# Optimization experiments

Hardware: AMD Instinct MI355X
Metric: run time of the kernel (lower is better)

## Reference

```python
import jax, jax.numpy as jnp
import numpy as np

B, N, F, E, D, H, L = 4, 2048, 2, 16, 32, 4, 2
GRAPH_LAYERS = 3
FLOW_ITERS = 10
COST_C = 1.0        # quadratic cost: c*x^2, inv_derivative(y) = y/(2c)
BIG_NUMBER = 1e7


def setup_inputs():
    key = jax.random.key(0)
    ks = jax.random.split(key, 20)
    node_features = jax.random.normal(ks[0], (B, N, F), jnp.float32)
    node_embeddings = jax.random.normal(ks[1], (B, N, E), jnp.float32)
    demands = jax.random.normal(ks[2], (B, N, 1), jnp.float32)
    demands = demands - demands.mean(axis=1, keepdims=True)  # flow conservation
    adj = (jax.random.uniform(ks[3], (B, N, N)) < 0.01).astype(jnp.float32)
    adj = adj * (1.0 - jnp.eye(N, dtype=jnp.float32))
    eye = jnp.broadcast_to(jnp.eye(N, dtype=jnp.float32), (B, N, N))
    neighborhoods = jnp.stack([eye, adj], axis=1)  # [B,L,N,N] hop-0 and hop-1
    def g(k, shape):
        return jax.random.normal(k, shape, jnp.float32) * 0.1
    params = {
        'We1': g(ks[4], (E + F, D)), 'be1': jnp.zeros((D,), jnp.float32),
        'We2': g(ks[5], (D, D)), 'be2': jnp.zeros((D,), jnp.float32),
        'w_attn': g(ks[6], (H, D)),
        'Wo': g(ks[7], (D, D)), 'bo': jnp.zeros((D,), jnp.float32),
        'Wz': g(ks[8], (D, D)), 'Uz': g(ks[9], (D, D)), 'bz': jnp.zeros((D,), jnp.float32),
        'Wr': g(ks[10], (D, D)), 'Ur': g(ks[11], (D, D)), 'br': jnp.zeros((D,), jnp.float32),
        'Wh': g(ks[12], (D, D)), 'Uh': g(ks[13], (D, D)), 'bh': jnp.zeros((D,), jnp.float32),
        'Wd1': g(ks[14], (D, D)), 'bd1': jnp.zeros((D,), jnp.float32),
        'Wd2': g(ks[15], (D, 1)), 'bd2': jnp.zeros((1,), jnp.float32),
        'Wv1': g(ks[16], (D, D)), 'bv1': jnp.zeros((D,), jnp.float32),
        'Wv2': g(ks[17], (D, 1)), 'bv2': jnp.zeros((1,), jnp.float32),
    }
    return {'node_features': node_features, 'node_embeddings': node_embeddings,
            'demands': demands, 'adj': adj, 'neighborhoods': neighborhoods, **params}


def _forward(node_features, node_embeddings, demands, adj, neighborhoods,
             We1, be1, We2, be2, w_attn, Wo, bo,
             Wz, Uz, bz, Wr, Ur, br, Wh, Uh, bh,
             Wd1, bd1, Wd2, bd2, Wv1, bv1, Wv2, bv2):
    # --- node encoder MLP (tanh, activate_final=True) ---
    x = jnp.concatenate([node_embeddings, node_features], axis=-1)   # [B,N,E+F]
    enc = jnp.tanh(jnp.tanh(x @ We1 + be1) @ We2 + be2)               # [B,N,D]
    # row-normalized neighborhood operators (degree-normalized aggregation)
    Mnorm = neighborhoods / (jnp.sum(neighborhoods, axis=-1, keepdims=True) + 1.0)
    # --- graph_layers x (attention neighborhood + GRU state update) ---
    for _ in range(GRAPH_LAYERS):
        agg = jnp.einsum('blnm,bmd->blnd', Mnorm, enc)                # [B,L,N,D]
        scores = jnp.einsum('blnd,hd->bhnl', jnp.tanh(agg), w_attn)   # [B,H,N,L]
        alpha = jax.nn.softmax(scores, axis=-1)
        ctx = jnp.einsum('bhnl,blnd->bnd', alpha, agg) / H            # mean over heads
        nbr = jnp.tanh(ctx @ Wo + bo)                                 # [B,N,D]
        z = jax.nn.sigmoid(nbr @ Wz + enc @ Uz + bz)
        r = jax.nn.sigmoid(nbr @ Wr + enc @ Ur + br)
        h = jnp.tanh(nbr @ Wh + (r * enc) @ Uh + bh)
        enc = z * enc + (1.0 - z) * h
    # --- primal: edge weights, masked softmax, proportional flow solver ---
    pred = (enc @ Wd1 + bd1) @ Wd2 + bd2                              # [B,N,1]
    pw = pred * jnp.transpose(pred, (0, 2, 1))                        # [B,N,N]
    weights = -BIG_NUMBER * (1.0 - adj) + pw
    fwp = jax.nn.softmax(weights, axis=-1)                            # rows sum to 1
    flow0 = fwp * jax.nn.relu(-demands)

    def step(flow, _):
        inflow = jnp.sum(flow, axis=1)[..., None]                     # [B,N,1]
        return fwp * jax.nn.relu(inflow - demands), None

    flow, _ = jax.lax.scan(step, flow0, None, length=FLOW_ITERS)
    flow_cost = jnp.sum(COST_C * flow * flow, axis=(1, 2))            # [B]
    # --- dual: dual variables, dual flows via inverse cost derivative ---
    dual = (enc @ Wv1 + bv1) @ Wv2 + bv2                              # [B,N,1]
    dd = dual - jnp.transpose(dual, (0, 2, 1))                        # [B,N,N]
    df = adj * jax.nn.relu(dd / (2.0 * COST_C))
    dual_cost = jnp.sum(COST_C * df * df - dd * df, axis=(1, 2)) \
        - jnp.sum(dual * demands, axis=(1, 2))                        # [B]
    return flow_cost - dual_cost                                      # primal-dual gap loss, [B]


def reference(node_features, node_embeddings, demands, adj, neighborhoods,
              We1, be1, We2, be2, w_attn, Wo, bo,
              Wz, Uz, bz, Wr, Ur, br, Wh, Uh, bh,
              Wd1, bd1, Wd2, bd2, Wv1, bv1, Wv2, bv2):
    return _forward(node_features, node_embeddings, demands, adj, neighborhoods,
                    We1, be1, We2, be2, w_attn, Wo, bo,
                    Wz, Uz, bz, Wr, Ur, br, Wh, Uh, bh,
                    Wd1, bd1, Wd2, bd2, Wv1, bv1, Wv2, bv2)
```

## Files before the change

kernel.cpp:

```cpp
#include <hip/hip_runtime.h>

#define NN 2048
#define NB 4
#define BN (NB * NN)
#define MAXD 96

__global__ __launch_bounds__(256) void k_front(
    const float* __restrict__ feat, const float* __restrict__ emb,
    const float* __restrict__ We1, const float* __restrict__ be1,
    const float* __restrict__ We2, const float* __restrict__ be2,
    float* __restrict__ enc_out,
    const float* __restrict__ adj, int* __restrict__ deg, int* __restrict__ cols,
    int* __restrict__ tdeg)
{
    int tid = threadIdx.x;
    if (blockIdx.x < 1024) {
        __shared__ float sW1[18 * 32], sb1[32], sW2[32 * 32], sb2[32];
        for (int i = tid; i < 18 * 32; i += 256) sW1[i] = We1[i];
        for (int i = tid; i < 32 * 32; i += 256) sW2[i] = We2[i];
        if (tid < 32) { sb1[tid] = be1[tid]; sb2[tid] = be2[tid]; }
        __syncthreads();
        int group = tid >> 5, j = tid & 31;
        int node = blockIdx.x * 8 + group;
        float x;
        if (j < 16)      x = emb[node * 16 + j];
        else if (j < 18) x = feat[node * 2 + (j - 16)];
        else             x = 0.f;
        float acc = sb1[j];
#pragma unroll
        for (int k = 0; k < 18; k++)
            acc += __shfl(x, k, 32) * sW1[k * 32 + j];
        float h = tanhf(acc);
        float acc2 = sb2[j];
#pragma unroll
        for (int k = 0; k < 32; k++)
            acc2 += __shfl(h, k, 32) * sW2[k * 32 + j];
        enc_out[node * 32 + j] = tanhf(acc2);
    } else {
        int wave = tid >> 6, lane = tid & 63;
        int row = (blockIdx.x - 1024) * 4 + wave;
        const float4* p = (const float4*)(adj + (size_t)row * NN);
        int cnt = 0;
        int base = row * MAXD;
#pragma unroll
        for (int it = 0; it < 8; it++) {
            float4 v = p[it * 64 + lane];
            float va[4] = { v.x, v.y, v.z, v.w };
#pragma unroll
            for (int c = 0; c < 4; c++) {
                unsigned long long m = __ballot(va[c] != 0.f);
                if (va[c] != 0.f) {
                    int pos = cnt + __popcll(m & ((1ull << lane) - 1ull));
                    if (pos < MAXD) cols[base + pos] = it * 256 + lane * 4 + c;
                }
                cnt += __popcll(m);
            }
        }
        if (lane == 0) {
            deg[row] = cnt < MAXD ? cnt : MAXD;
            tdeg[row] = 0;
        }
    }
}

__device__ __forceinline__ float layer_body(
    int node, int j, int d, const int* __restrict__ cp,
    const float* __restrict__ encB, float e,
    const float* sAttn, const float* sWo, const float* sbo,
    const float* sWz, const float* sUz, const float* sbz,
    const float* sWr, const float* sUr, const float* sbr,
    const float* sWh, const float* sUh, const float* sbh)
{
    float agg0 = 0.5f * e;
    int iA = cp[j];
    int iB = cp[j + 32];
    float a1 = 0.f, a1b = 0.f;
    int dmin = d < 32 ? d : 32;
#pragma unroll 4
    for (int i = 0; i < dmin - 1; i += 2) {
        int m0 = __shfl(iA, i, 32);
        int m1 = __shfl(iA, i + 1, 32);
        a1  += encB[m0 * 32 + j];
        a1b += encB[m1 * 32 + j];
    }
    if (dmin & 1) { int m = __shfl(iA, dmin - 1, 32); a1 += encB[m * 32 + j]; }
#pragma unroll 2
    for (int i = 32; i < d; i++) {
        int m = __shfl(iB, i - 32, 32);
        a1 += encB[m * 32 + j];
    }
    a1 = (a1 + a1b) * (1.0f / (float)(d + 1));
    float t0 = tanhf(agg0), t1 = tanhf(a1);
    float sc[8];
#pragma unroll
    for (int h2 = 0; h2 < 4; h2++) { sc[h2] = sAttn[h2 * 32 + j] * t0; sc[4 + h2] = sAttn[h2 * 32 + j] * t1; }
#pragma unroll
    for (int off = 16; off >= 1; off >>= 1)
#pragma unroll
        for (int q = 0; q < 8; q++) sc[q] += __shfl_xor(sc[q], off, 32);
    float c0 = 0.f, c1 = 0.f;
#pragma unroll
    for (int h2 = 0; h2 < 4; h2++) {
        float a = sc[h2], bsc = sc[4 + h2];
        float mx = fmaxf(a, bsc);
        float e0 = expf(a - mx), e1 = expf(bsc - mx);
        float inv = 1.0f / (e0 + e1);
        c0 += e0 * inv; c1 += e1 * inv;
    }
    c0 *= 0.25f; c1 *= 0.25f;
    float ctx = c0 * agg0 + c1 * a1;
    float acc = sbo[j];
#pragma unroll
    for (int k = 0; k < 32; k++) acc += __shfl(ctx, k, 32) * sWo[k * 32 + j];
    float nbr = tanhf(acc);
    float az = sbz[j], ar = sbr[j], ah = sbh[j];
#pragma unroll
    for (int k = 0; k < 32; k++) {
        float nb = __shfl(nbr, k, 32);
        float en = __shfl(e, k, 32);
        az += nb * sWz[k * 32 + j] + en * sUz[k * 32 + j];
        ar += nb * sWr[k * 32 + j] + en * sUr[k * 32 + j];
        ah += nb * sWh[k * 32 + j];
    }
    float z = 1.0f / (1.0f + expf(-az));
    float r = 1.0f / (1.0f + expf(-ar));
    float re = r * e;
#pragma unroll
    for (int k = 0; k < 32; k++) ah += __shfl(re, k, 32) * sUh[k * 32 + j];
    float hc = tanhf(ah);
    return z * e + (1.0f - z) * hc;
}

__global__ __launch_bounds__(1024) void k_layer(
    const float* __restrict__ enc_in, float* __restrict__ enc_out,
    const int* __restrict__ deg, const int* __restrict__ cols,
    const float* __restrict__ w_attn,
    const float* __restrict__ Wo, const float* __restrict__ bo,
    const float* __restrict__ Wz, const float* __restrict__ Uz, const float* __restrict__ bz,
    const float* __restrict__ Wr, const float* __restrict__ Ur, const float* __restrict__ br,
    const float* __restrict__ Wh, const float* __restrict__ Uh, const float* __restrict__ bh)
{
    __shared__ float sWo[1024], sWz[1024], sUz[1024], sWr[1024], sUr[1024], sWh[1024], sUh[1024];
    __shared__ float sbo[32], sbz[32], sbr[32], sbh[32], sAttn[128];
    int tid = threadIdx.x;
    {
        int i = tid;
        sWo[i] = Wo[i]; sWz[i] = Wz[i]; sUz[i] = Uz[i];
        sWr[i] = Wr[i]; sUr[i] = Ur[i]; sWh[i] = Wh[i]; sUh[i] = Uh[i];
    }
    if (tid < 32) { sbo[tid] = bo[tid]; sbz[tid] = bz[tid]; sbr[tid] = br[tid]; sbh[tid] = bh[tid]; }
    if (tid < 128) sAttn[tid] = w_attn[tid];
    __syncthreads();
    int group = tid >> 5, j = tid & 31;
    int node = blockIdx.x * 32 + group;
    int b = node >> 11;
    const float* encB = enc_in + (size_t)(b * NN) * 32;
    float e = enc_in[node * 32 + j];
    int d = deg[node];
    const int* cp = cols + node * MAXD;
    float eo = layer_body(node, j, d, cp, encB, e, sAttn, sWo, sbo,
                          sWz, sUz, sbz, sWr, sUr, sbr, sWh, sUh, sbh);
    enc_out[node * 32 + j] = eo;
}

__global__ __launch_bounds__(1024) void k_layer_last(
    const float* __restrict__ enc_in,
    const int* __restrict__ deg, const int* __restrict__ cols,
    const float* __restrict__ w_attn,
    const float* __restrict__ Wo, const float* __restrict__ bo,
    const float* __restrict__ Wz, const float* __restrict__ Uz, const float* __restrict__ bz,
    const float* __restrict__ Wr, const float* __restrict__ Ur, const float* __restrict__ br,
    const float* __restrict__ Wh, const float* __restrict__ Uh, const float* __restrict__ bh,
    const float* __restrict__ Wd1, const float* __restrict__ bd1,
    const float* __restrict__ Wd2, const float* __restrict__ bd2,
    const float* __restrict__ Wv1, const float* __restrict__ bv1,
    const float* __restrict__ Wv2, const float* __restrict__ bv2,
    float* __restrict__ pred, float* __restrict__ dual)
{
    __shared__ float sWo[1024], sWz[1024], sUz[1024], sWr[1024], sUr[1024], sWh[1024], sUh[1024];
    __shared__ float sWd1[1024], sWv1[1024];
    __shared__ float sbo[32], sbz[32], sbr[32], sbh[32], sAttn[128];
    __shared__ float sbd1[32], sbv1[32], sWd2[32], sWv2[32];
    int tid = threadIdx.x;
    {
        int i = tid;
        sWo[i] = Wo[i]; sWz[i] = Wz[i]; sUz[i] = Uz[i];
        sWr[i] = Wr[i]; sUr[i] = Ur[i]; sWh[i] = Wh[i]; sUh[i] = Uh[i];
        sWd1[i] = Wd1[i]; sWv1[i] = Wv1[i];
    }
    if (tid < 32) {
        sbo[tid] = bo[tid]; sbz[tid] = bz[tid]; sbr[tid] = br[tid]; sbh[tid] = bh[tid];
        sbd1[tid] = bd1[tid]; sbv1[tid] = bv1[tid]; sWd2[tid] = Wd2[tid]; sWv2[tid] = Wv2[tid];
    }
    if (tid < 128) sAttn[tid] = w_attn[tid];
    __syncthreads();
    int group = tid >> 5, j = tid & 31;
    int node = blockIdx.x * 32 + group;
    int b = node >> 11;
    const float* encB = enc_in + (size_t)(b * NN) * 32;
    float e = enc_in[node * 32 + j];
    int d = deg[node];
    const int* cp = cols + node * MAXD;
    float eo = layer_body(node, j, d, cp, encB, e, sAttn, sWo, sbo,
                          sWz, sUz, sbz, sWr, sUr, sbr, sWh, sUh, sbh);
    float ad = sbd1[j], av = sbv1[j];
#pragma unroll
    for (int k = 0; k < 32; k++) {
        float en = __shfl(eo, k, 32);
        ad += en * sWd1[k * 32 + j];
        av += en * sWv1[k * 32 + j];
    }
    float pd = ad * sWd2[j];
    float dv = av * sWv2[j];
#pragma unroll
    for (int off = 16; off >= 1; off >>= 1) {
        pd += __shfl_xor(pd, off, 32);
        dv += __shfl_xor(dv, off, 32);
    }
    if (j == 0) {
        pred[node] = pd + bd2[0];
        dual[node] = dv + bv2[0];
    }
}

__global__ __launch_bounds__(256) void k_edge_scatter(
    const int* __restrict__ deg, const int* __restrict__ cols,
    const float* __restrict__ pred, const float* __restrict__ dual,
    int* __restrict__ tdeg, unsigned* __restrict__ tpack,
    float* __restrict__ rowsq, float* __restrict__ rowdual)
{
    int wave = threadIdx.x >> 6, lane = threadIdx.x & 63;
    int row = blockIdx.x * 4 + wave;
    int b = row >> 11;
    int rloc = row & (NN - 1);
    const float* predB = pred + b * NN;
    const float* dualB = dual + b * NN;
    int d = deg[row];
    int base = row * MAXD;
    float pn = pred[row];
    float dn = dual[row];
    float mx = -1e30f;
    for (int i = lane; i < d; i += 64) {
        int c = cols[base + i];
        mx = fmaxf(mx, pn * predB[c]);
    }
#pragma unroll
    for (int off = 32; off >= 1; off >>= 1) mx = fmaxf(mx, __shfl_xor(mx, off));
    float den = 0.f, du = 0.f;
    for (int i = lane; i < d; i += 64) {
        int c = cols[base + i];
        den += expf(pn * predB[c] - mx);
        float dd = dn - dualB[c];
        if (dd > 0.f) du -= 0.25f * dd * dd;
    }
#pragma unroll
    for (int off = 32; off >= 1; off >>= 1) { den += __shfl_xor(den, off); du += __shfl_xor(du, off); }
    float invden = 1.0f / den;
    float rs = 0.f;
    for (int i = lane; i < d; i += 64) {
        int c = cols[base + i];
        float f = expf(pn * predB[c] - mx) * invden;
        rs += f * f;
        int pos = atomicAdd(&tdeg[b * NN + c], 1);
        if (pos < MAXD) {
            unsigned wv = ((__float_as_uint(f) + 0x400u) & 0xFFFFF800u) | (unsigned)rloc;
            tpack[(size_t)(b * MAXD + pos) * NN + c] = wv;
        }
    }
#pragma unroll
    for (int off = 32; off >= 1; off >>= 1) rs += __shfl_xor(rs, off);
    if (lane == 0) { rowsq[row] = rs; rowdual[row] = du; }
}

__global__ __launch_bounds__(1024) void k_flow_batch(
    const int* __restrict__ tdeg, const unsigned* __restrict__ tpack,
    const float* __restrict__ demands,
    const float* __restrict__ rowsq, const float* __restrict__ rowdual,
    const float* __restrict__ dual, float* __restrict__ out)
{
    __shared__ float sdem[NN], sA[NN], sBuf[NN];
    __shared__ float red[3][16];
    int tid = threadIdx.x;
    int b = blockIdx.x;
    const float* demB = demands + b * NN;
    for (int n = tid; n < NN; n += 1024) {
        float dm = demB[n];
        sdem[n] = dm;
        sA[n] = fmaxf(-dm, 0.f);
    }
    __syncthreads();
    int n0 = tid, n1 = tid + 1024;
    int d0 = tdeg[b * NN + n0];
    int d1 = tdeg[b * NN + n1];
    const unsigned* tp = tpack + (size_t)b * MAXD * NN;
#pragma unroll 1
    for (int it = 0; it < 5; it++) {
        {
            float a0 = 0.f, a1 = 0.f;
            for (int i = 0; i < d0; i++) {
                unsigned wv = tp[i * NN + n0];
                a0 += __uint_as_float(wv & 0xFFFFF800u) * sA[wv & 0x7FFu];
            }
            for (int i = 0; i < d1; i++) {
                unsigned wv = tp[i * NN + n1];
                a1 += __uint_as_float(wv & 0xFFFFF800u) * sA[wv & 0x7FFu];
            }
            sBuf[n0] = fmaxf(a0 - sdem[n0], 0.f);
            sBuf[n1] = fmaxf(a1 - sdem[n1], 0.f);
        }
        __syncthreads();
        {
            float a0 = 0.f, a1 = 0.f;
            for (int i = 0; i < d0; i++) {
                unsigned wv = tp[i * NN + n0];
                a0 += __uint_as_float(wv & 0xFFFFF800u) * sBuf[wv & 0x7FFu];
            }
            for (int i = 0; i < d1; i++) {
                unsigned wv = tp[i * NN + n1];
                a1 += __uint_as_float(wv & 0xFFFFF800u) * sBuf[wv & 0x7FFu];
            }
            sA[n0] = fmaxf(a0 - sdem[n0], 0.f);
            sA[n1] = fmaxf(a1 - sdem[n1], 0.f);
        }
        __syncthreads();
    }
    float fc = 0.f, ds = 0.f, dq = 0.f;
    for (int n = tid; n < NN; n += 1024) {
        int row = b * NN + n;
        float sv = sA[n];
        fc += rowsq[row] * sv * sv;
        ds += rowdual[row];
        dq += dual[row] * sdem[n];
    }
#pragma unroll
    for (int off = 32; off >= 1; off >>= 1) {
        fc += __shfl_xor(fc, off);
        ds += __shfl_xor(ds, off);
        dq += __shfl_xor(dq, off);
    }
    int wv = tid >> 6;
    if ((tid & 63) == 0) { red[0][wv] = fc; red[1][wv] = ds; red[2][wv] = dq; }
    __syncthreads();
    if (tid == 0) {
        float a = 0.f, s1 = 0.f, s2 = 0.f;
        for (int w = 0; w < 16; w++) { a += red[0][w]; s1 += red[1][w]; s2 += red[2][w]; }
        out[b] = a - s1 + s2;
    }
}

extern "C" void kernel_launch(void* const* d_in, const int* in_sizes, int n_in,
                              void* d_out, int out_size, void* d_ws, size_t ws_size,
                              hipStream_t stream) {
    const float* feat = (const float*)d_in[0];
    const float* emb  = (const float*)d_in[1];
    const float* dem  = (const float*)d_in[2];
    const float* adj  = (const float*)d_in[3];
    const float* We1 = (const float*)d_in[5];
    const float* be1 = (const float*)d_in[6];
    const float* We2 = (const float*)d_in[7];
    const float* be2 = (const float*)d_in[8];
    const float* w_attn = (const float*)d_in[9];
    const float* Wo = (const float*)d_in[10];
    const float* bo = (const float*)d_in[11];
    const float* Wz = (const float*)d_in[12];
    const float* Uz = (const float*)d_in[13];
    const float* bz = (const float*)d_in[14];
    const float* Wr = (const float*)d_in[15];
    const float* Ur = (const float*)d_in[16];
    const float* br = (const float*)d_in[17];
    const float* Wh = (const float*)d_in[18];
    const float* Uh = (const float*)d_in[19];
    const float* bh = (const float*)d_in[20];
    const float* Wd1 = (const float*)d_in[21];
    const float* bd1 = (const float*)d_in[22];
    const float* Wd2 = (const float*)d_in[23];
    const float* bd2 = (const float*)d_in[24];
    const float* Wv1 = (const float*)d_in[25];
    const float* bv1 = (const float*)d_in[26];
    const float* Wv2 = (const float*)d_in[27];
    const float* bv2 = (const float*)d_in[28];
    float* out = (float*)d_out;

    float* w = (float*)d_ws;
    float* enc0 = w;            w += (size_t)BN * 32;
    float* enc1 = w;            w += (size_t)BN * 32;
    int*   degp = (int*)w;      w += BN;
    int*   colp = (int*)w;      w += (size_t)BN * MAXD;
    float* pred = w;            w += BN;
    float* dual = w;            w += BN;
    float* rowsq = w;           w += BN;
    float* rowdual = w;         w += BN;
    int*   tdeg = (int*)w;      w += BN;
    unsigned* tpk = (unsigned*)w; w += (size_t)BN * MAXD;

    k_front<<<3072, 256, 0, stream>>>(feat, emb, We1, be1, We2, be2, enc0,
                                      adj, degp, colp, tdeg);
    k_layer<<<BN / 32, 1024, 0, stream>>>(enc0, enc1, degp, colp, w_attn,
                                          Wo, bo, Wz, Uz, bz, Wr, Ur, br, Wh, Uh, bh);
    k_layer<<<BN / 32, 1024, 0, stream>>>(enc1, enc0, degp, colp, w_attn,
                                          Wo, bo, Wz, Uz, bz, Wr, Ur, br, Wh, Uh, bh);
    k_layer_last<<<BN / 32, 1024, 0, stream>>>(enc0, degp, colp, w_attn,
                                               Wo, bo, Wz, Uz, bz, Wr, Ur, br, Wh, Uh, bh,
                                               Wd1, bd1, Wd2, bd2, Wv1, bv1, Wv2, bv2,
                                               pred, dual);
    k_edge_scatter<<<BN / 4, 256, 0, stream>>>(degp, colp, pred, dual,
                                               tdeg, tpk, rowsq, rowdual);
    k_flow_batch<<<NB, 1024, 0, stream>>>(tdeg, tpk, dem,
                                          rowsq, rowdual, dual, out);
}
```

Baseline: 406.8 us.

## Use fast math intrinsics, sigmoid-form attention, and packed shared-memory weights in GNN layers

Replaces tanhf/expf/division with exp-based tanh, __expf and hardware reciprocal throughout. Rewrites the two-way attention softmax as a sigmoid of the score difference, which halves the reductions. Broadcasts neighbour indices, context and gate inputs through shared memory instead of wave shuffles, and packs the GRU weights into float4/float2 so fewer LDS loads are needed. The cost is lower numerical accuracy from the approximate math and extra shared-memory traffic and footprint per block.

```diff
diff --git a/kernel.cpp b/kernel.cpp
--- a/kernel.cpp
+++ b/kernel.cpp
@@ -4,6 +4,16 @@
 #define NB 4
 #define BN (NB * NN)
 #define MAXD 96
+
+__device__ __forceinline__ float fast_rcp(float x) { return __builtin_amdgcn_rcpf(x); }
+__device__ __forceinline__ float fast_tanh(float x) {
+    float a = __expf(2.0f * fabsf(x));
+    float r = 1.0f - 2.0f * fast_rcp(1.0f + a);
+    return copysignf(r, x);
+}
+__device__ __forceinline__ float fast_sigmoid(float x) {
+    return fast_rcp(1.0f + __expf(-x));
+}
 
 __global__ __launch_bounds__(256) void k_front(
     const float* __restrict__ feat, const float* __restrict__ emb,
@@ -30,12 +40,12 @@
 #pragma unroll
         for (int k = 0; k < 18; k++)
             acc += __shfl(x, k, 32) * sW1[k * 32 + j];
-        float h = tanhf(acc);
+        float h = fast_tanh(acc);
         float acc2 = sb2[j];
 #pragma unroll
         for (int k = 0; k < 32; k++)
             acc2 += __shfl(h, k, 32) * sW2[k * 32 + j];
-        enc_out[node * 32 + j] = tanhf(acc2);
+        enc_out[node * 32 + j] = fast_tanh(acc2);
     } else {
         int wave = tid >> 6, lane = tid & 63;
         int row = (blockIdx.x - 1024) * 4 + wave;
@@ -63,71 +73,66 @@
     }
 }
 
-__device__ __forceinline__ float layer_body(
-    int node, int j, int d, const int* __restrict__ cp,
+__device__ __forceinline__ float layer_body2(
+    int g, int j, int d, const int* __restrict__ cp,
     const float* __restrict__ encB, float e,
-    const float* sAttn, const float* sWo, const float* sbo,
-    const float* sWz, const float* sUz, const float* sbz,
-    const float* sWr, const float* sUr, const float* sbr,
-    const float* sWh, const float* sUh, const float* sbh)
-{
-    float agg0 = 0.5f * e;
-    int iA = cp[j];
-    int iB = cp[j + 32];
+    const float4* sPack, const float2* sWhUh, const float* sWo,
+    const float* sAttn, const float* sbo, const float* sbz,
+    const float* sbr, const float* sbh,
+    int (*sCols)[64], float2 (*sNE)[32], float (*sCtx)[32])
+{
+    sCols[g][j]      = cp[j];
+    sCols[g][j + 32] = cp[j + 32];
     float a1 = 0.f, a1b = 0.f;
-    int dmin = d < 32 ? d : 32;
-#pragma unroll 4
-    for (int i = 0; i < dmin - 1; i += 2) {
-        int m0 = __shfl(iA, i, 32);
-        int m1 = __shfl(iA, i + 1, 32);
+    int i = 0;
+#pragma unroll 2
+    for (; i + 1 < d; i += 2) {
+        int m0 = sCols[g][i], m1 = sCols[g][i + 1];
         a1  += encB[m0 * 32 + j];
         a1b += encB[m1 * 32 + j];
     }
-    if (dmin & 1) { int m = __shfl(iA, dmin - 1, 32); a1 += encB[m * 32 + j]; }
-#pragma unroll 2
-    for (int i = 32; i < d; i++) {
-        int m = __shfl(iB, i - 32, 32);
-        a1 += encB[m * 32 + j];
-    }
-    a1 = (a1 + a1b) * (1.0f / (float)(d + 1));
-    float t0 = tanhf(agg0), t1 = tanhf(a1);
-    float sc[8];
-#pragma unroll
-    for (int h2 = 0; h2 < 4; h2++) { sc[h2] = sAttn[h2 * 32 + j] * t0; sc[4 + h2] = sAttn[h2 * 32 + j] * t1; }
-#pragma unroll
-    for (int off = 16; off >= 1; off >>= 1)
-#pragma unroll
-        for (int q = 0; q < 8; q++) sc[q] += __shfl_xor(sc[q], off, 32);
-    float c0 = 0.f, c1 = 0.f;
-#pragma unroll
-    for (int h2 = 0; h2 < 4; h2++) {
-        float a = sc[h2], bsc = sc[4 + h2];
-        float mx = fmaxf(a, bsc);
-        float e0 = expf(a - mx), e1 = expf(bsc - mx);
-        float inv = 1.0f / (e0 + e1);
-        c0 += e0 * inv; c1 += e1 * inv;
-    }
-    c0 *= 0.25f; c1 *= 0.25f;
-    float ctx = c0 * agg0 + c1 * a1;
+    if (i < d) a1 += encB[sCols[g][i] * 32 + j];
+    float agg0 = 0.5f * e;
+    a1 = (a1 + a1b) * fast_rcp((float)(d + 1));
+    float t0 = fast_tanh(agg0), t1 = fast_tanh(a1);
+    float td = t0 - t1;
+    float s0 = sAttn[j] * td, s1 = sAttn[32 + j] * td,
+          s2 = sAttn[64 + j] * td, s3 = sAttn[96 + j] * td;
+#pragma unroll
+    for (int off = 16; off >= 1; off >>= 1) {
+        s0 += __shfl_xor(s0, off, 32);
+        s1 += __shfl_xor(s1, off, 32);
+        s2 += __shfl_xor(s2, off, 32);
+        s3 += __shfl_xor(s3, off, 32);
+    }
+    float c0 = 0.25f * (fast_sigmoid(s0) + fast_sigmoid(s1) +
+                        fast_sigmoid(s2) + fast_sigmoid(s3));
+    float ctx = c0 * agg0 + (1.0f - c0) * a1;
+    sCtx[g][j] = ctx;
     float acc = sbo[j];
 #pragma unroll
-    for (int k = 0; k < 32; k++) acc += __shfl(ctx, k, 32) * sWo[k * 32 + j];
-    float nbr = tanhf(acc);
-    float az = sbz[j], ar = sbr[j], ah = sbh[j];
+    for (int k = 0; k < 32; k++)
+        acc += sCtx[g][k] * sWo[k * 32 + j];
+    float nbr = fast_tanh(acc);
+    sNE[g][j] = make_float2(nbr, e);
+    float az = sbz[j], ar = sbr[j];
 #pragma unroll
     for (int k = 0; k < 32; k++) {
-        float nb = __shfl(nbr, k, 32);
-        float en = __shfl(e, k, 32);
-        az += nb * sWz[k * 32 + j] + en * sUz[k * 32 + j];
-        ar += nb * sWr[k * 32 + j] + en * sUr[k * 32 + j];
-        ah += nb * sWh[k * 32 + j];
-    }
-    float z = 1.0f / (1.0f + expf(-az));
-    float r = 1.0f / (1.0f + expf(-ar));
-    float re = r * e;
-#pragma unroll
-    for (int k = 0; k < 32; k++) ah += __shfl(re, k, 32) * sUh[k * 32 + j];
-    float hc = tanhf(ah);
+        float2 ne = sNE[g][k];
+        float4 w  = sPack[k * 32 + j];
+        az += ne.x * w.x + ne.y * w.y;
+        ar += ne.x * w.z + ne.y * w.w;
+    }
+    float z = fast_sigmoid(az), r = fast_sigmoid(ar);
+    sNE[g][j].y = r * e;
+    float ah = sbh[j];
+#pragma unroll
+    for (int k = 0; k < 32; k++) {
+        float2 ne = sNE[g][k];
+        float2 wh = sWhUh[k * 32 + j];
+        ah += ne.x * wh.x + ne.y * wh.y;
+    }
+    float hc = fast_tanh(ah);
     return z * e + (1.0f - z) * hc;
 }
 
@@ -140,26 +145,29 @@
     const float* __restrict__ Wr, const float* __restrict__ Ur, const float* __restrict__ br,
     const float* __restrict__ Wh, const float* __restrict__ Uh, const float* __restrict__ bh)
 {
-    __shared__ float sWo[1024], sWz[1024], sUz[1024], sWr[1024], sUr[1024], sWh[1024], sUh[1024];
-    __shared__ float sbo[32], sbz[32], sbr[32], sbh[32], sAttn[128];
+    __shared__ float4 sPack[1024];
+    __shared__ float2 sWhUh[1024];
+    __shared__ float  sWo[1024];
+    __shared__ float  sAttn[128], sbo[32], sbz[32], sbr[32], sbh[32];
+    __shared__ int    sCols[32][64];
+    __shared__ float2 sNE[32][32];
+    __shared__ float  sCtx[32][32];
     int tid = threadIdx.x;
-    {
-        int i = tid;
-        sWo[i] = Wo[i]; sWz[i] = Wz[i]; sUz[i] = Uz[i];
-        sWr[i] = Wr[i]; sUr[i] = Ur[i]; sWh[i] = Wh[i]; sUh[i] = Uh[i];
-    }
+    sPack[tid] = make_float4(Wz[tid], Uz[tid], Wr[tid], Ur[tid]);
+    sWhUh[tid] = make_float2(Wh[tid], Uh[tid]);
+    sWo[tid] = Wo[tid];
+    if (tid < 128) sAttn[tid] = w_attn[tid];
     if (tid < 32) { sbo[tid] = bo[tid]; sbz[tid] = bz[tid]; sbr[tid] = br[tid]; sbh[tid] = bh[tid]; }
-    if (tid < 128) sAttn[tid] = w_attn[tid];
     __syncthreads();
-    int group = tid >> 5, j = tid & 31;
-    int node = blockIdx.x * 32 + group;
+    int g = tid >> 5, j = tid & 31;
+    int node = blockIdx.x * 32 + g;
     int b = node >> 11;
     const float* encB = enc_in + (size_t)(b * NN) * 32;
     float e = enc_in[node * 32 + j];
     int d = deg[node];
     const int* cp = cols + node * MAXD;
-    float eo = layer_body(node, j, d, cp, encB, e, sAttn, sWo, sbo,
-                          sWz, sUz, sbz, sWr, sUr, sbr, sWh, sUh, sbh);
+    float eo = layer_body2(g, j, d, cp, encB, e, sPack, sWhUh, sWo,
+                           sAttn, sbo, sbz, sbr, sbh, sCols, sNE, sCtx);
     enc_out[node * 32 + j] = eo;
 }
 
@@ -177,41 +185,46 @@
     const float* __restrict__ Wv2, const float* __restrict__ bv2,
     float* __restrict__ pred, float* __restrict__ dual)
 {
-    __shared__ float sWo[1024], sWz[1024], sUz[1024], sWr[1024], sUr[1024], sWh[1024], sUh[1024];
-    __shared__ float sWd1[1024], sWv1[1024];
-    __shared__ float sbo[32], sbz[32], sbr[32], sbh[32], sAttn[128];
-    __shared__ float sbd1[32], sbv1[32], sWd2[32], sWv2[32];
+    __shared__ float4 sPack[1024];
+    __shared__ float2 sWhUh[1024];
+    __shared__ float2 sWdv[1024];
+    __shared__ float  sWo[1024];
+    __shared__ float  sAttn[128], sbo[32], sbz[32], sbr[32], sbh[32];
+    __shared__ float  sbd1[32], sbv1[32], sWd2v[32], sWv2v[32];
+    __shared__ int    sCols[32][64];
+    __shared__ float2 sNE[32][32];
+    __shared__ float  sCtx[32][32];
     int tid = threadIdx.x;
-    {
-        int i = tid;
-        sWo[i] = Wo[i]; sWz[i] = Wz[i]; sUz[i] = Uz[i];
-        sWr[i] = Wr[i]; sUr[i] = Ur[i]; sWh[i] = Wh[i]; sUh[i] = Uh[i];
-        sWd1[i] = Wd1[i]; sWv1[i] = Wv1[i];
-    }
+    sPack[tid] = make_float4(Wz[tid], Uz[tid], Wr[tid], Ur[tid]);
+    sWhUh[tid] = make_float2(Wh[tid], Uh[tid]);
+    sWdv[tid]  = make_float2(Wd1[tid], Wv1[tid]);
+    sWo[tid] = Wo[tid];
+    if (tid < 128) sAttn[tid] = w_attn[tid];
     if (tid < 32) {
         sbo[tid] = bo[tid]; sbz[tid] = bz[tid]; sbr[tid] = br[tid]; sbh[tid] = bh[tid];
-        sbd1[tid] = bd1[tid]; sbv1[tid] = bv1[tid]; sWd2[tid] = Wd2[tid]; sWv2[tid] = Wv2[tid];
-    }
-    if (tid < 128) sAttn[tid] = w_attn[tid];
+        sbd1[tid] = bd1[tid]; sbv1[tid] = bv1[tid]; sWd2v[tid] = Wd2[tid]; sWv2v[tid] = Wv2[tid];
+    }
     __syncthreads();
-    int group = tid >> 5, j = tid & 31;
-    int node = blockIdx.x * 32 + group;
+    int g = tid >> 5, j = tid & 31;
+    int node = blockIdx.x * 32 + g;
     int b = node >> 11;
     const float* encB = enc_in + (size_t)(b * NN) * 32;
     float e = enc_in[node * 32 + j];
     int d = deg[node];
     const int* cp = cols + node * MAXD;
-    float eo = layer_body(node, j, d, cp, encB, e, sAttn, sWo, sbo,
-                          sWz, sUz, sbz, sWr, sUr, sbr, sWh, sUh, sbh);
+    float eo = layer_body2(g, j, d, cp, encB, e, sPack, sWhUh, sWo,
+                           sAttn, sbo, sbz, sbr, sbh, sCols, sNE, sCtx);
+    sCtx[g][j] = eo;
     float ad = sbd1[j], av = sbv1[j];
 #pragma unroll
     for (int k = 0; k < 32; k++) {
-        float en = __shfl(eo, k, 32);
-        ad += en * sWd1[k * 32 + j];
-        av += en * sWv1[k * 32 + j];
-    }
-    float pd = ad * sWd2[j];
-    float dv = av * sWv2[j];
+        float ek = sCtx[g][k];
+        float2 wd = sWdv[k * 32 + j];
+        ad += ek * wd.x;
+        av += ek * wd.y;
+    }
+    float pd = ad * sWd2v[j];
+    float dv = av * sWv2v[j];
 #pragma unroll
     for (int off = 16; off >= 1; off >>= 1) {
         pd += __shfl_xor(pd, off, 32);
@@ -249,17 +262,17 @@
     float den = 0.f, du = 0.f;
     for (int i = lane; i < d; i += 64) {
         int c = cols[base + i];
-        den += expf(pn * predB[c] - mx);
+        den += __expf(pn * predB[c] - mx);
         float dd = dn - dualB[c];
         if (dd > 0.f) du -= 0.25f * dd * dd;
     }
 #pragma unroll
     for (int off = 32; off >= 1; off >>= 1) { den += __shfl_xor(den, off); du += __shfl_xor(du, off); }
-    float invden = 1.0f / den;
+    float invden = fast_rcp(den);
     float rs = 0.f;
     for (int i = lane; i < d; i += 64) {
         int c = cols[base + i];
-        float f = expf(pn * predB[c] - mx) * invden;
+        float f = __expf(pn * predB[c] - mx) * invden;
         rs += f * f;
         int pos = atomicAdd(&tdeg[b * NN + c], 1);
         if (pos < MAXD) {
```

New measurement: 387.9 us. 4.6% less time.
